# Performance work log

Hardware: AMD Instinct MI355X
Metric: run time of the kernel (lower is better)

## Reference

```python
import jax, jax.numpy as jnp
import numpy as np

N = 50000      # nodes
E = 600000     # edges
G = 512        # graphs in batch
H = 128        # hidden_dim
F_IN = 4       # node_features
ED = 2         # edge_dim
OUT = 256      # output_dim
L = 7          # conv layers 1..7 (layer 0 is separate: 4->128 with residual)
EPS = 1e-5     # BatchNorm eps


def setup_inputs() -> dict:
    key = jax.random.key(0)
    ks = jax.random.split(key, 32)
    rn = lambda k, shape, s=0.05: jax.random.normal(k, shape, dtype=jnp.float32) * s
    inp = {}
    inp["x"] = jax.random.normal(ks[0], (N, F_IN), dtype=jnp.float32)
    inp["edge_attr"] = jax.random.normal(ks[1], (E, ED), dtype=jnp.float32)
    # layer 0: EdgeUpdateConv(4, 128) with residual projection
    inp["We0"] = rn(ks[2], (F_IN + ED, H)); inp["be0"] = rn(ks[3], (H,))
    inp["Wn0"] = rn(ks[4], (H, H));        inp["bno0"] = rn(ks[5], (H,))
    inp["g0"] = jnp.ones((H,), jnp.float32); inp["bt0"] = jnp.zeros((H,), jnp.float32)
    inp["m0"] = rn(ks[6], (H,)); inp["v0"] = jax.random.uniform(ks[7], (H,), dtype=jnp.float32) + 0.5
    inp["Wr0"] = rn(ks[8], (F_IN, H)); inp["br0"] = rn(ks[9], (H,))
    # layers 1..7: EdgeUpdateConv(128, 128), stacked params
    inp["We_s"] = rn(ks[10], (L, H + ED, H)); inp["be_s"] = rn(ks[11], (L, H))
    inp["Wn_s"] = rn(ks[12], (L, H, H));      inp["bno_s"] = rn(ks[13], (L, H))
    inp["g_s"] = jnp.ones((L, H), jnp.float32); inp["bt_s"] = jnp.zeros((L, H), jnp.float32)
    inp["m_s"] = rn(ks[14], (L, H)); inp["v_s"] = jax.random.uniform(ks[15], (L, H), dtype=jnp.float32) + 0.5
    # head
    inp["W1"] = rn(ks[16], (2 * H, H)); inp["b1"] = rn(ks[17], (H,))
    inp["g1"] = jnp.ones((H,), jnp.float32); inp["bt1"] = jnp.zeros((H,), jnp.float32)
    inp["m1"] = rn(ks[18], (H,)); inp["v1"] = jax.random.uniform(ks[19], (H,), dtype=jnp.float32) + 0.5
    inp["W2"] = rn(ks[20], (H, OUT)); inp["b2"] = rn(ks[21], (OUT,))
    # int inputs
    inp["edge_index"] = jax.random.randint(ks[22], (2, E), 0, N, dtype=jnp.int32)
    inp["batch"] = jnp.sort(jax.random.randint(ks[23], (N,), 0, G, dtype=jnp.int32))
    return inp


def _bn(x, g, b, m, v):
    # eval-mode BatchNorm1d
    return (x - m) * (g * jax.lax.rsqrt(v + EPS)) + b


def reference(x, edge_attr, We0, be0, Wn0, bno0, g0, bt0, m0, v0, Wr0, br0,
              We_s, be_s, Wn_s, bno_s, g_s, bt_s, m_s, v_s,
              W1, b1, g1, bt1, m1, v1, W2, b2, edge_index, batch):
    src, dst = edge_index[0], edge_index[1]
    # in-degree for mean aggregation (isolated nodes -> 0 output, guard /0)
    deg = jnp.maximum(jax.ops.segment_sum(jnp.ones((E,), jnp.float32), dst, num_segments=N), 1.0)

    def conv(h, We, be, Wn, bno, g, bt, m, v, res):
        # message: gather x_j, concat edge_attr, linear_edge  -> [E, H]
        msg = jnp.concatenate([h[src], edge_attr], axis=1) @ We + be
        # scatter-mean aggregate -> [N, H]
        agg = jax.ops.segment_sum(msg, dst, num_segments=N) / deg[:, None]
        # update: linear_node, then BN, residual, ReLU
        out = _bn(agg @ Wn + bno, g, bt, m, v)
        return jax.nn.relu(out + res)

    h = conv(x, We0, be0, Wn0, bno0, g0, bt0, m0, v0, x @ Wr0 + br0)
    for i in range(L):  # fixed small layer loop
        h = conv(h, We_s[i], be_s[i], Wn_s[i], bno_s[i], g_s[i], bt_s[i], m_s[i], v_s[i], h)

    # global mean / max pooling per graph
    ones_n = jnp.ones((N,), jnp.float32)
    cnt = jnp.maximum(jax.ops.segment_sum(ones_n, batch, num_segments=G), 1.0)
    mean_p = jax.ops.segment_sum(h, batch, num_segments=G) / cnt[:, None]
    max_p = jax.ops.segment_max(h, batch, num_segments=G)
    z = jnp.concatenate([mean_p, max_p], axis=1)  # [G, 2H]
    z = jax.nn.relu(_bn(z @ W1 + b1, g1, bt1, m1, v1))
    z = z @ W2 + b2
    return z / jnp.maximum(jnp.linalg.norm(z, axis=1, keepdims=True), 1e-12)
```

## Files before the change

### kernel.cpp

```cpp
#include <hip/hip_runtime.h>

constexpr int NN   = 50000;
constexpr int NPAD = 50016;
constexpr int NE   = 600000;
constexpr int NG   = 512;
constexpr int HD   = 128;
constexpr float BN_EPS = 1e-5f;
constexpr int CWS  = HD*HD + 2*HD + HD;
constexpr int WMF_L = 2*4*4*128*8;

typedef __attribute__((ext_vector_type(8))) short bf16x8;
typedef __attribute__((ext_vector_type(4))) float f32x4;

__device__ inline unsigned short bf16rne(float v) {
  unsigned u = __float_as_uint(v);
  return (unsigned short)((u + 0x7FFFu + ((u >> 16) & 1u)) >> 16);
}
__device__ inline void bfsplit(float v, unsigned short& h, unsigned short& l) {
  unsigned short hb = bf16rne(v);
  float hf = __uint_as_float((unsigned)hb << 16);
  l = bf16rne(v - hf);
  h = hb;
}
__device__ inline float blo(unsigned u) { return __uint_as_float(u << 16); }
__device__ inline float bhi(unsigned u) { return __uint_as_float(u & 0xFFFF0000u); }


__global__ __launch_bounds__(256) void k_deg(const int* __restrict__ ei,
                                             int* __restrict__ deg, int* __restrict__ rank) {
  int e = blockIdx.x * 256 + threadIdx.x;
  if (e >= NE) return;
  rank[e] = atomicAdd(&deg[ei[NE + e]], 1);
}

__global__ __launch_bounds__(1024) void k_scanA(const int* __restrict__ deg,
                                                int* __restrict__ rowptr, int* __restrict__ bsum) {
  __shared__ int sm[1024];
  int t = threadIdx.x, b = blockIdx.x;
  int i = b * 1024 + t;
  int v = (i < NN) ? deg[i] : 0;
  sm[t] = v;
  __syncthreads();
  for (int off = 1; off < 1024; off <<= 1) {
    int add = (t >= off) ? sm[t - off] : 0;
    __syncthreads();
    sm[t] += add;
    __syncthreads();
  }
  int incl = sm[t];
  if (i < NN) rowptr[i] = incl - v;
  if (t == 1023) bsum[b] = incl;
}

__global__ __launch_bounds__(1024) void k_scanC(int* rowptr, const int* __restrict__ bsum) {
  __shared__ int base;
  int b = blockIdx.x;
  if (threadIdx.x == 0) {
    int acc = 0;
    for (int j = 0; j < b; j++) acc += bsum[j];
    base = acc;
    if (b == 0) rowptr[NN] = NE;
  }
  __syncthreads();
  int i = b * 1024 + threadIdx.x;
  if (i < NN) rowptr[i] += base;
}

__global__ __launch_bounds__(256) void k_scatter(
    const int* __restrict__ ei, const float* __restrict__ ea, const int* __restrict__ rowptr,
    const int* __restrict__ rank, int* __restrict__ csr, float* __restrict__ eap) {
  int e = blockIdx.x * 256 + threadIdx.x;
  if (e >= NE) return;
  int s = ei[e], d = ei[NE + e];
  int pos = rowptr[d] + rank[e];
  csr[pos] = s;
  *(float2*)(eap + 2 * (size_t)pos) = *(const float2*)(ea + 2 * (size_t)e);
}

__global__ __launch_bounds__(128) void k_combine(
    const float* __restrict__ We0, const float* __restrict__ be0, const float* __restrict__ Wn0,
    const float* __restrict__ We_s, const float* __restrict__ be_s, const float* __restrict__ Wn_s,
    float* __restrict__ cw, unsigned short* __restrict__ wmf) {
  int l = blockIdx.x / 131;
  int r = blockIdx.x % 131;
  int j = threadIdx.x;
  float* slot = cw + (size_t)l * CWS;
  const float* Wn;
  const float* Arow;
  float* dst;
  if (l == 0) {
    Wn = Wn0;
    if (r < 4)       { Arow = We0 + r * HD; dst = slot + r * HD; }
    else if (r < 6)  { Arow = We0 + r * HD; dst = slot + HD * HD + (r - 4) * HD; }
    else if (r == 6) { Arow = be0;          dst = slot + HD * HD + 2 * HD; }
    else return;
  } else {
    int li = l - 1;
    Wn = Wn_s + (size_t)li * HD * HD;
    const float* We = We_s + (size_t)li * 130 * HD;
    if (r < 128)      { Arow = We + r * HD;  dst = slot + r * HD; }
    else if (r < 130) { Arow = We + r * HD;  dst = slot + HD * HD + (r - 128) * HD; }
    else              { Arow = be_s + li * HD; dst = slot + HD * HD + 2 * HD; }
  }
  float acc = 0.f;
  for (int t = 0; t < HD; t++) acc = fmaf(Arow[t], Wn[t * HD + j], acc);
  dst[j] = acc;
  if (l >= 1 && r < 128) {
    unsigned short hb, lb;
    bfsplit(acc, hb, lb);
    size_t wbase = (size_t)(l - 1) * WMF_L;
    int kb = r >> 5, ks2 = (r >> 3) & 3, jj = r & 7;
    size_t o = (size_t)((kb * 4 + ks2) * 128 + j) * 8 + jj;
    wmf[wbase + o] = hb;
    wmf[wbase + WMF_L / 2 + o] = lb;
  }
}

__global__ __launch_bounds__(256) void k_node0(
    const int* __restrict__ rowptr, const int* __restrict__ csr, const float* __restrict__ eap,
    const float* __restrict__ x, const int* __restrict__ deg, const float* __restrict__ cw0,
    const float* __restrict__ bno0, const float* __restrict__ g0, const float* __restrict__ bt0,
    const float* __restrict__ m0, const float* __restrict__ v0,
    const float* __restrict__ Wr0, const float* __restrict__ br0,
    float* __restrict__ Se, unsigned short* __restrict__ outHi, unsigned short* __restrict__ outLo) {
  int g32 = threadIdx.x >> 5;
  int i = blockIdx.x * 8 + g32;
  if (i >= NN) return;
  int l = threadIdx.x & 31;
  int e0 = rowptr[i], e1 = rowptr[i + 1];
  float sx0 = 0.f, sx1 = 0.f, sx2 = 0.f, sx3 = 0.f, se0 = 0.f, se1 = 0.f;
  for (int e = e0 + l; e < e1; e += 32) {
    int s = csr[e];
    float4 xv = *(const float4*)(x + 4 * (size_t)s);
    sx0 += xv.x; sx1 += xv.y; sx2 += xv.z; sx3 += xv.w;
    float2 ev = *(const float2*)(eap + 2 * (size_t)e);
    se0 += ev.x; se1 += ev.y;
  }
#pragma unroll
  for (int m = 1; m <= 16; m <<= 1) {
    sx0 += __shfl_xor(sx0, m); sx1 += __shfl_xor(sx1, m);
    sx2 += __shfl_xor(sx2, m); sx3 += __shfl_xor(sx3, m);
    se0 += __shfl_xor(se0, m); se1 += __shfl_xor(se1, m);
  }
  if (l == 0) *(float2*)(Se + 2 * (size_t)i) = make_float2(se0, se1);
  float dg = (float)deg[i];
  float dgi = 1.0f / fmaxf(dg, 1.0f);
  float4 xr = *(const float4*)(x + 4 * (size_t)i);
  const float* Wc0  = cw0;
  const float* wce0 = cw0 + HD * HD;
  const float* bc0  = cw0 + HD * HD + 2 * HD;
  ushort4 hs, ls;
  unsigned short* hp = (unsigned short*)&hs;
  unsigned short* lp = (unsigned short*)&ls;
#pragma unroll
  for (int k2 = 0; k2 < 4; k2++) {
    int c = l * 4 + k2;
    float y = sx0 * Wc0[c] + sx1 * Wc0[HD + c] + sx2 * Wc0[2 * HD + c] + sx3 * Wc0[3 * HD + c];
    y += se0 * wce0[c] + se1 * wce0[HD + c] + dg * bc0[c];
    y = y * dgi + bno0[c];
    float sc = g0[c] * rsqrtf(v0[c] + BN_EPS);
    y = (y - m0[c]) * sc + bt0[c];
    float r = br0[c] + xr.x * Wr0[c] + xr.y * Wr0[HD + c] + xr.z * Wr0[2 * HD + c] + xr.w * Wr0[3 * HD + c];
    float o = fmaxf(y + r, 0.f);
    bfsplit(o, hp[k2], lp[k2]);
  }
  *(ushort4*)(outHi + (size_t)i * HD + l * 4) = hs;
  *(ushort4*)(outLo + (size_t)i * HD + l * 4) = ls;
}


__global__ __launch_bounds__(256, 8) void k_layer(
    const unsigned short* __restrict__ hHi, const unsigned short* __restrict__ hLo,
    const int* __restrict__ rowptr, const int* __restrict__ csr,
    const float* __restrict__ cwl, const unsigned short* __restrict__ wmf,
    const float* __restrict__ bno, const float* __restrict__ gam, const float* __restrict__ bet,
    const float* __restrict__ mu, const float* __restrict__ var,
    const float* __restrict__ Se, const int* __restrict__ deg,
    unsigned short* __restrict__ outHi, unsigned short* __restrict__ outLo) {
  __shared__ unsigned short St_hi[32 * 136];
  __shared__ unsigned short St_lo[32 * 136];
  int tid = threadIdx.x;
  int wid = tid >> 6, lane = tid & 63;
  int half = lane >> 5, l5 = lane & 31;
  int rowbase = blockIdx.x * 32;
  const uint2* hb2 = (const uint2*)hHi;

#pragma unroll
  for (int rp = 0; rp < 4; rp++) {
    int lr = wid * 8 + rp * 2 + half;
    int i = rowbase + lr;
    int e = 0, e1 = 0;
    if (i < NN) { e = rowptr[i]; e1 = rowptr[i + 1]; }
    float a0 = 0.f, a1 = 0.f, a2 = 0.f, a3 = 0.f;
    for (; e + 3 < e1; e += 4) {
      int s0 = csr[e], s1 = csr[e + 1], s2 = csr[e + 2], s3 = csr[e + 3];
      uint2 v0 = hb2[(size_t)s0 * 32 + l5];
      uint2 v1 = hb2[(size_t)s1 * 32 + l5];
      uint2 v2 = hb2[(size_t)s2 * 32 + l5];
      uint2 v3 = hb2[(size_t)s3 * 32 + l5];
      a0 += blo(v0.x) + blo(v1.x) + blo(v2.x) + blo(v3.x);
      a1 += bhi(v0.x) + bhi(v1.x) + bhi(v2.x) + bhi(v3.x);
      a2 += blo(v0.y) + blo(v1.y) + blo(v2.y) + blo(v3.y);
      a3 += bhi(v0.y) + bhi(v1.y) + bhi(v2.y) + bhi(v3.y);
    }
    if (e + 1 < e1) {
      int s0 = csr[e], s1 = csr[e + 1];
      uint2 v0 = hb2[(size_t)s0 * 32 + l5];
      uint2 v1 = hb2[(size_t)s1 * 32 + l5];
      a0 += blo(v0.x) + blo(v1.x); a1 += bhi(v0.x) + bhi(v1.x);
      a2 += blo(v0.y) + blo(v1.y); a3 += bhi(v0.y) + bhi(v1.y);
      e += 2;
    }
    if (e < e1) {
      uint2 v = hb2[(size_t)csr[e] * 32 + l5];
      a0 += blo(v.x); a1 += bhi(v.x); a2 += blo(v.y); a3 += bhi(v.y);
    }
    unsigned short h0, l0, h1, l1, h2, l2, h3, l3;
    bfsplit(a0, h0, l0); bfsplit(a1, h1, l1); bfsplit(a2, h2, l2); bfsplit(a3, h3, l3);
    *(ushort4*)&St_hi[lr * 136 + l5 * 4] = make_ushort4(h0, h1, h2, h3);
    *(ushort4*)&St_lo[lr * 136 + l5 * 4] = make_ushort4(l0, l1, l2, l3);
  }
  __syncthreads();

  int wm = wid >> 1, wn = wid & 1;
  int nlane = lane & 15, ksub = lane >> 4;
  const unsigned short* wh = wmf;
  const unsigned short* wl = wmf + WMF_L / 2;
  f32x4 acc[4];
#pragma unroll
  for (int nt = 0; nt < 4; nt++) acc[nt] = (f32x4){0.f, 0.f, 0.f, 0.f};
  int arow = wm * 16 + nlane;
#pragma unroll
  for (int ks = 0; ks < 4; ks++) {
    bf16x8 ah = *(const bf16x8*)&St_hi[arow * 136 + ks * 32 + ksub * 8];
    bf16x8 al = *(const bf16x8*)&St_lo[arow * 136 + ks * 32 + ksub * 8];
#pragma unroll
    for (int nt = 0; nt < 4; nt++) {
      int col = wn * 64 + nt * 16 + nlane;
      bf16x8 bh = *(const bf16x8*)&wh[(size_t)((ks * 4 + ksub) * 128 + col) * 8];
      bf16x8 bl = *(const bf16x8*)&wl[(size_t)((ks * 4 + ksub) * 128 + col) * 8];
      acc[nt] = __builtin_amdgcn_mfma_f32_16x16x32_bf16(ah, bh, acc[nt], 0, 0, 0);
      acc[nt] = __builtin_amdgcn_mfma_f32_16x16x32_bf16(al, bh, acc[nt], 0, 0, 0);
      acc[nt] = __builtin_amdgcn_mfma_f32_16x16x32_bf16(ah, bl, acc[nt], 0, 0, 0);
    }
  }

  const float* wce = cwl + HD * HD;
  const float* bcp = cwl + HD * HD + 2 * HD;
  int rb = wm * 16 + ksub * 4;
  float dgv[4], dgiv[4];
  float2 sevv[4];
#pragma unroll
  for (int i2 = 0; i2 < 4; i2++) {
    size_t row = (size_t)rowbase + rb + i2;
    float dg = (float)deg[row];
    dgv[i2] = dg;
    dgiv[i2] = 1.0f / fmaxf(dg, 1.0f);
    sevv[i2] = *(const float2*)(Se + row * 2);
  }
#pragma unroll
  for (int nt = 0; nt < 4; nt++) {
    int col = wn * 64 + nt * 16 + nlane;
    float w0 = wce[col], w1 = wce[HD + col], bcv = bcp[col], bnov = bno[col];
    float sc = gam[col] * rsqrtf(var[col] + BN_EPS);
    float sh = bet[col] - mu[col] * sc;
#pragma unroll
    for (int i2 = 0; i2 < 4; i2++) {
      size_t row = (size_t)rowbase + rb + i2;
      size_t idx = row * HD + col;
      float res = __uint_as_float((unsigned)hHi[idx] << 16)
                + __uint_as_float((unsigned)hLo[idx] << 16);
      float y = (acc[nt][i2] + sevv[i2].x * w0 + sevv[i2].y * w1 + dgv[i2] * bcv) * dgiv[i2] + bnov;
      y = fmaxf(y * sc + sh + res, 0.f);
      unsigned short yh, yl;
      bfsplit(y, yh, yl);
      outHi[idx] = yh;
      outLo[idx] = yl;
    }
  }
}


__global__ __launch_bounds__(512) void k_pool(
    const unsigned short* __restrict__ hb, const int* __restrict__ batch,
    float* __restrict__ meanp, float* __restrict__ maxp) {
  __shared__ float ssum[512], smax[512];
  int g = blockIdx.x, t = threadIdx.x;
  int d = t & 127, sub = t >> 7;
  int lo = 0, hi = NN;
  while (lo < hi) { int mid = (lo + hi) >> 1; if (batch[mid] < g) lo = mid + 1; else hi = mid; }
  int start = lo;
  lo = start; hi = NN;
  while (lo < hi) { int mid = (lo + hi) >> 1; if (batch[mid] < g + 1) lo = mid + 1; else hi = mid; }
  int end = lo;
  float sum = 0.f, mx = -3.4e38f;
  for (int i = start + sub; i < end; i += 4) {
    float val = __uint_as_float((unsigned)hb[(size_t)i * HD + d] << 16);
    sum += val;
    mx = fmaxf(mx, val);
  }
  ssum[t] = sum; smax[t] = mx;
  __syncthreads();
  if (sub == 0) {
    sum = ssum[t] + ssum[t + 128] + ssum[t + 256] + ssum[t + 384];
    mx = fmaxf(fmaxf(smax[t], smax[t + 128]), fmaxf(smax[t + 256], smax[t + 384]));
    int cnt = end - start;
    meanp[g * HD + d] = sum / fmaxf((float)cnt, 1.f);
    maxp[g * HD + d] = (cnt > 0) ? mx : 0.f;
  }
}

__global__ __launch_bounds__(256) void k_head(
    const float* __restrict__ meanp, const float* __restrict__ maxp,
    const float* __restrict__ W1, const float* __restrict__ b1,
    const float* __restrict__ g1, const float* __restrict__ bt1,
    const float* __restrict__ m1, const float* __restrict__ v1,
    const float* __restrict__ W2, const float* __restrict__ b2,
    float* __restrict__ outp) {
  __shared__ float z[256];
  __shared__ float s1[128];
  __shared__ float red[256];
  int g = blockIdx.x, t = threadIdx.x;
  z[t] = (t < 128) ? meanp[g * HD + t] : maxp[g * HD + (t - 128)];
  __syncthreads();
  if (t < 128) {
    float y = b1[t];
    for (int k = 0; k < 256; k++) y = fmaf(z[k], W1[k * HD + t], y);
    float sc = g1[t] * rsqrtf(v1[t] + BN_EPS);
    y = (y - m1[t]) * sc + bt1[t];
    s1[t] = fmaxf(y, 0.f);
  }
  __syncthreads();
  float o = b2[t];
  for (int k = 0; k < 128; k++) o = fmaf(s1[k], W2[k * 256 + t], o);
  red[t] = o * o;
  __syncthreads();
  for (int off = 128; off > 0; off >>= 1) {
    if (t < off) red[t] += red[t + off];
    __syncthreads();
  }
  float scale = 1.0f / fmaxf(sqrtf(red[0]), 1e-12f);
  outp[(size_t)g * 256 + t] = o * scale;
}


extern "C" void kernel_launch(void* const* d_in, const int* in_sizes, int n_in,
                              void* d_out, int out_size, void* d_ws, size_t ws_size,
                              hipStream_t stream) {
  const float* x         = (const float*)d_in[0];
  const float* edge_attr = (const float*)d_in[1];
  const float* We0  = (const float*)d_in[2];
  const float* be0  = (const float*)d_in[3];
  const float* Wn0  = (const float*)d_in[4];
  const float* bno0 = (const float*)d_in[5];
  const float* g0   = (const float*)d_in[6];
  const float* bt0  = (const float*)d_in[7];
  const float* m0   = (const float*)d_in[8];
  const float* v0   = (const float*)d_in[9];
  const float* Wr0  = (const float*)d_in[10];
  const float* br0  = (const float*)d_in[11];
  const float* We_s = (const float*)d_in[12];
  const float* be_s = (const float*)d_in[13];
  const float* Wn_s = (const float*)d_in[14];
  const float* bno_s= (const float*)d_in[15];
  const float* g_s  = (const float*)d_in[16];
  const float* bt_s = (const float*)d_in[17];
  const float* m_s  = (const float*)d_in[18];
  const float* v_s  = (const float*)d_in[19];
  const float* W1   = (const float*)d_in[20];
  const float* b1   = (const float*)d_in[21];
  const float* g1   = (const float*)d_in[22];
  const float* bt1  = (const float*)d_in[23];
  const float* m1   = (const float*)d_in[24];
  const float* v1   = (const float*)d_in[25];
  const float* W2   = (const float*)d_in[26];
  const float* b2   = (const float*)d_in[27];
  const int* edge_index = (const int*)d_in[28];
  const int* batch      = (const int*)d_in[29];
  float* outp = (float*)d_out;

  char* ws = (char*)d_ws;
  size_t off = 0;
  auto alloc = [&](size_t bytes) -> void* {
    void* p = ws + off;
    off = (off + bytes + 255) & ~(size_t)255;
    return p;
  };
  unsigned short* hAHi = (unsigned short*)alloc((size_t)NPAD * HD * 2);
  unsigned short* hALo = (unsigned short*)alloc((size_t)NPAD * HD * 2);
  unsigned short* hBHi = (unsigned short*)alloc((size_t)NPAD * HD * 2);
  unsigned short* hBLo = (unsigned short*)alloc((size_t)NPAD * HD * 2);
  float* Se    = (float*)alloc((size_t)NPAD * 2 * 4);
  int*   deg   = (int*)alloc((size_t)NPAD * 4);
  int*   rowptr= (int*)alloc((size_t)(NN + 1) * 4);
  int*   rank  = (int*)alloc((size_t)NE * 4);
  int*   csr   = (int*)alloc((size_t)NE * 4);
  float* eap   = (float*)alloc((size_t)NE * 2 * 4);
  int*   bsum  = (int*)alloc(64 * 4);
  float* cw    = (float*)alloc((size_t)8 * CWS * 4);
  unsigned short* wmf = (unsigned short*)alloc((size_t)7 * WMF_L * 2);
  float* meanp = (float*)alloc((size_t)NG * HD * 4);
  float* maxp  = (float*)alloc((size_t)NG * HD * 4);
  (void)ws_size; (void)n_in; (void)in_sizes; (void)out_size;

  hipMemsetAsync(deg, 0, (size_t)NPAD * 4, stream);

  k_deg<<<(NE + 255) / 256, 256, 0, stream>>>(edge_index, deg, rank);
  k_scanA<<<49, 1024, 0, stream>>>(deg, rowptr, bsum);
  k_scanC<<<49, 1024, 0, stream>>>(rowptr, bsum);
  k_scatter<<<(NE + 255) / 256, 256, 0, stream>>>(edge_index, edge_attr, rowptr, rank, csr, eap);
  k_combine<<<8 * 131, 128, 0, stream>>>(We0, be0, Wn0, We_s, be_s, Wn_s, cw, wmf);
  k_node0<<<(NN + 7) / 8, 256, 0, stream>>>(rowptr, csr, eap, x, deg, cw,
                                            bno0, g0, bt0, m0, v0, Wr0, br0,
                                            Se, hAHi, hALo);

  unsigned short* curHi = hAHi; unsigned short* curLo = hALo;
  unsigned short* othHi = hBHi; unsigned short* othLo = hBLo;
  for (int l = 1; l <= 7; ++l) {
    int li = l - 1;
    k_layer<<<NPAD / 32, 256, 0, stream>>>(curHi, curLo, rowptr, csr,
        cw + (size_t)l * CWS, wmf + (size_t)li * WMF_L,
        bno_s + li * HD, g_s + li * HD, bt_s + li * HD, m_s + li * HD, v_s + li * HD,
        Se, deg, othHi, othLo);
    unsigned short* t;
    t = curHi; curHi = othHi; othHi = t;
    t = curLo; curLo = othLo; othLo = t;
  }

  k_pool<<<NG, 512, 0, stream>>>(curHi, batch, meanp, maxp);
  k_head<<<NG, 256, 0, stream>>>(meanp, maxp, W1, b1, g1, bt1, m1, v1, W2, b2, outp);
}
```

Baseline: 538.0 us.

## Halve layer tile rows, fuse deg with combine and pool with head

The layer kernel now processes 16 rows per block instead of 32. Each of the four waves owns a 32-column slice of a single 16-row MFMA tile, which doubles the block count to improve load balance on the gather phase. The degree-count kernel and the weight-combine kernel are merged into one launch, and pooling is merged with the MLP head, removing two launches and the intermediate mean/max buffers. The trade-off is that each block reloads the weight fragments for fewer rows, so weight reuse per block drops.

```diff
diff --git a/kernel.cpp b/kernel.cpp
--- a/kernel.cpp
+++ b/kernel.cpp
@@ -8,6 +8,10 @@
 constexpr float BN_EPS = 1e-5f;
 constexpr int CWS  = HD*HD + 2*HD + HD;
 constexpr int WMF_L = 2*4*4*128*8;
+constexpr int TR   = 16;
+constexpr int DEG_BLOCKS = (NE + 255) / 256;
+constexpr int CMB_UNITS  = 8 * 131;
+constexpr int CMB_BLOCKS = CMB_UNITS / 2;
 
 typedef __attribute__((ext_vector_type(8))) short bf16x8;
 typedef __attribute__((ext_vector_type(4))) float f32x4;
@@ -26,64 +30,19 @@
 __device__ inline float bhi(unsigned u) { return __uint_as_float(u & 0xFFFF0000u); }
 
 
-__global__ __launch_bounds__(256) void k_deg(const int* __restrict__ ei,
-                                             int* __restrict__ deg, int* __restrict__ rank) {
-  int e = blockIdx.x * 256 + threadIdx.x;
-  if (e >= NE) return;
-  rank[e] = atomicAdd(&deg[ei[NE + e]], 1);
-}
-
-__global__ __launch_bounds__(1024) void k_scanA(const int* __restrict__ deg,
-                                                int* __restrict__ rowptr, int* __restrict__ bsum) {
-  __shared__ int sm[1024];
-  int t = threadIdx.x, b = blockIdx.x;
-  int i = b * 1024 + t;
-  int v = (i < NN) ? deg[i] : 0;
-  sm[t] = v;
-  __syncthreads();
-  for (int off = 1; off < 1024; off <<= 1) {
-    int add = (t >= off) ? sm[t - off] : 0;
-    __syncthreads();
-    sm[t] += add;
-    __syncthreads();
-  }
-  int incl = sm[t];
-  if (i < NN) rowptr[i] = incl - v;
-  if (t == 1023) bsum[b] = incl;
-}
-
-__global__ __launch_bounds__(1024) void k_scanC(int* rowptr, const int* __restrict__ bsum) {
-  __shared__ int base;
-  int b = blockIdx.x;
-  if (threadIdx.x == 0) {
-    int acc = 0;
-    for (int j = 0; j < b; j++) acc += bsum[j];
-    base = acc;
-    if (b == 0) rowptr[NN] = NE;
-  }
-  __syncthreads();
-  int i = b * 1024 + threadIdx.x;
-  if (i < NN) rowptr[i] += base;
-}
-
-__global__ __launch_bounds__(256) void k_scatter(
-    const int* __restrict__ ei, const float* __restrict__ ea, const int* __restrict__ rowptr,
-    const int* __restrict__ rank, int* __restrict__ csr, float* __restrict__ eap) {
-  int e = blockIdx.x * 256 + threadIdx.x;
-  if (e >= NE) return;
-  int s = ei[e], d = ei[NE + e];
-  int pos = rowptr[d] + rank[e];
-  csr[pos] = s;
-  *(float2*)(eap + 2 * (size_t)pos) = *(const float2*)(ea + 2 * (size_t)e);
-}
-
-__global__ __launch_bounds__(128) void k_combine(
+__global__ __launch_bounds__(256) void k_deg_combine(
+    const int* __restrict__ ei, int* __restrict__ deg, int* __restrict__ rank,
     const float* __restrict__ We0, const float* __restrict__ be0, const float* __restrict__ Wn0,
     const float* __restrict__ We_s, const float* __restrict__ be_s, const float* __restrict__ Wn_s,
     float* __restrict__ cw, unsigned short* __restrict__ wmf) {
-  int l = blockIdx.x / 131;
-  int r = blockIdx.x % 131;
-  int j = threadIdx.x;
+  int b = blockIdx.x;
+  if (b < DEG_BLOCKS) {
+    int e = b * 256 + threadIdx.x;
+    if (e < NE) rank[e] = atomicAdd(&deg[ei[NE + e]], 1);
+    return;
+  }
+  int u = (b - DEG_BLOCKS) * 2 + (threadIdx.x >> 7);
+  int l = u / 131, r = u % 131, j = threadIdx.x & 127;
   float* slot = cw + (size_t)l * CWS;
   const float* Wn;
   const float* Arow;
@@ -114,6 +73,51 @@
     wmf[wbase + o] = hb;
     wmf[wbase + WMF_L / 2 + o] = lb;
   }
+}
+
+
+__global__ __launch_bounds__(1024) void k_scanA(const int* __restrict__ deg,
+                                                int* __restrict__ rowptr, int* __restrict__ bsum) {
+  __shared__ int sm[1024];
+  int t = threadIdx.x, b = blockIdx.x;
+  int i = b * 1024 + t;
+  int v = (i < NN) ? deg[i] : 0;
+  sm[t] = v;
+  __syncthreads();
+  for (int off = 1; off < 1024; off <<= 1) {
+    int add = (t >= off) ? sm[t - off] : 0;
+    __syncthreads();
+    sm[t] += add;
+    __syncthreads();
+  }
+  int incl = sm[t];
+  if (i < NN) rowptr[i] = incl - v;
+  if (t == 1023) bsum[b] = incl;
+}
+
+__global__ __launch_bounds__(1024) void k_scanC(int* rowptr, const int* __restrict__ bsum) {
+  __shared__ int base;
+  int b = blockIdx.x;
+  if (threadIdx.x == 0) {
+    int acc = 0;
+    for (int j = 0; j < b; j++) acc += bsum[j];
+    base = acc;
+    if (b == 0) rowptr[NN] = NE;
+  }
+  __syncthreads();
+  int i = b * 1024 + threadIdx.x;
+  if (i < NN) rowptr[i] += base;
+}
+
+__global__ __launch_bounds__(256) void k_scatter(
+    const int* __restrict__ ei, const float* __restrict__ ea, const int* __restrict__ rowptr,
+    const int* __restrict__ rank, int* __restrict__ csr, float* __restrict__ eap) {
+  int e = blockIdx.x * 256 + threadIdx.x;
+  if (e >= NE) return;
+  int s = ei[e], d = ei[NE + e];
+  int pos = rowptr[d] + rank[e];
+  csr[pos] = s;
+  *(float2*)(eap + 2 * (size_t)pos) = *(const float2*)(ea + 2 * (size_t)e);
 }
 
 __global__ __launch_bounds__(256) void k_node0(
@@ -177,17 +181,17 @@
     const float* __restrict__ mu, const float* __restrict__ var,
     const float* __restrict__ Se, const int* __restrict__ deg,
     unsigned short* __restrict__ outHi, unsigned short* __restrict__ outLo) {
-  __shared__ unsigned short St_hi[32 * 136];
-  __shared__ unsigned short St_lo[32 * 136];
+  __shared__ unsigned short St_hi[TR * 136];
+  __shared__ unsigned short St_lo[TR * 136];
   int tid = threadIdx.x;
   int wid = tid >> 6, lane = tid & 63;
   int half = lane >> 5, l5 = lane & 31;
-  int rowbase = blockIdx.x * 32;
+  int rowbase = blockIdx.x * TR;
   const uint2* hb2 = (const uint2*)hHi;
 
 #pragma unroll
-  for (int rp = 0; rp < 4; rp++) {
-    int lr = wid * 8 + rp * 2 + half;
+  for (int rp = 0; rp < 2; rp++) {
+    int lr = wid * 4 + rp * 2 + half;
     int i = rowbase + lr;
     int e = 0, e1 = 0;
     if (i < NN) { e = rowptr[i]; e1 = rowptr[i + 1]; }
@@ -222,21 +226,19 @@
   }
   __syncthreads();
 
-  int wm = wid >> 1, wn = wid & 1;
   int nlane = lane & 15, ksub = lane >> 4;
   const unsigned short* wh = wmf;
   const unsigned short* wl = wmf + WMF_L / 2;
-  f32x4 acc[4];
-#pragma unroll
-  for (int nt = 0; nt < 4; nt++) acc[nt] = (f32x4){0.f, 0.f, 0.f, 0.f};
-  int arow = wm * 16 + nlane;
+  f32x4 acc[2];
+#pragma unroll
+  for (int nt = 0; nt < 2; nt++) acc[nt] = (f32x4){0.f, 0.f, 0.f, 0.f};
 #pragma unroll
   for (int ks = 0; ks < 4; ks++) {
-    bf16x8 ah = *(const bf16x8*)&St_hi[arow * 136 + ks * 32 + ksub * 8];
-    bf16x8 al = *(const bf16x8*)&St_lo[arow * 136 + ks * 32 + ksub * 8];
-#pragma unroll
-    for (int nt = 0; nt < 4; nt++) {
-      int col = wn * 64 + nt * 16 + nlane;
+    bf16x8 ah = *(const bf16x8*)&St_hi[nlane * 136 + ks * 32 + ksub * 8];
+    bf16x8 al = *(const bf16x8*)&St_lo[nlane * 136 + ks * 32 + ksub * 8];
+#pragma unroll
+    for (int nt = 0; nt < 2; nt++) {
+      int col = wid * 32 + nt * 16 + nlane;
       bf16x8 bh = *(const bf16x8*)&wh[(size_t)((ks * 4 + ksub) * 128 + col) * 8];
       bf16x8 bl = *(const bf16x8*)&wl[(size_t)((ks * 4 + ksub) * 128 + col) * 8];
       acc[nt] = __builtin_amdgcn_mfma_f32_16x16x32_bf16(ah, bh, acc[nt], 0, 0, 0);
@@ -247,7 +249,7 @@
 
   const float* wce = cwl + HD * HD;
   const float* bcp = cwl + HD * HD + 2 * HD;
-  int rb = wm * 16 + ksub * 4;
+  int rb = ksub * 4;
   float dgv[4], dgiv[4];
   float2 sevv[4];
 #pragma unroll
@@ -259,8 +261,8 @@
     sevv[i2] = *(const float2*)(Se + row * 2);
   }
 #pragma unroll
-  for (int nt = 0; nt < 4; nt++) {
-    int col = wn * 64 + nt * 16 + nlane;
+  for (int nt = 0; nt < 2; nt++) {
+    int col = wid * 32 + nt * 16 + nlane;
     float w0 = wce[col], w1 = wce[HD + col], bcv = bcp[col], bnov = bno[col];
     float sc = gam[col] * rsqrtf(var[col] + BN_EPS);
     float sh = bet[col] - mu[col] * sc;
@@ -281,10 +283,17 @@
 }
 
 
-__global__ __launch_bounds__(512) void k_pool(
+__global__ __launch_bounds__(512) void k_poolhead(
     const unsigned short* __restrict__ hb, const int* __restrict__ batch,
-    float* __restrict__ meanp, float* __restrict__ maxp) {
+    const float* __restrict__ W1, const float* __restrict__ b1,
+    const float* __restrict__ g1, const float* __restrict__ bt1,
+    const float* __restrict__ m1, const float* __restrict__ v1,
+    const float* __restrict__ W2, const float* __restrict__ b2,
+    float* __restrict__ outp) {
   __shared__ float ssum[512], smax[512];
+  __shared__ float pmean[128], pmax[128];
+  __shared__ float s1[128];
+  __shared__ float red[512];
   int g = blockIdx.x, t = threadIdx.x;
   int d = t & 127, sub = t >> 7;
   int lo = 0, hi = NN;
@@ -305,42 +314,32 @@
     sum = ssum[t] + ssum[t + 128] + ssum[t + 256] + ssum[t + 384];
     mx = fmaxf(fmaxf(smax[t], smax[t + 128]), fmaxf(smax[t + 256], smax[t + 384]));
     int cnt = end - start;
-    meanp[g * HD + d] = sum / fmaxf((float)cnt, 1.f);
-    maxp[g * HD + d] = (cnt > 0) ? mx : 0.f;
-  }
-}
-
-__global__ __launch_bounds__(256) void k_head(
-    const float* __restrict__ meanp, const float* __restrict__ maxp,
-    const float* __restrict__ W1, const float* __restrict__ b1,
-    const float* __restrict__ g1, const float* __restrict__ bt1,
-    const float* __restrict__ m1, const float* __restrict__ v1,
-    const float* __restrict__ W2, const float* __restrict__ b2,
-    float* __restrict__ outp) {
-  __shared__ float z[256];
-  __shared__ float s1[128];
-  __shared__ float red[256];
-  int g = blockIdx.x, t = threadIdx.x;
-  z[t] = (t < 128) ? meanp[g * HD + t] : maxp[g * HD + (t - 128)];
+    pmean[d] = sum / fmaxf((float)cnt, 1.f);
+    pmax[d] = (cnt > 0) ? mx : 0.f;
+  }
   __syncthreads();
   if (t < 128) {
     float y = b1[t];
-    for (int k = 0; k < 256; k++) y = fmaf(z[k], W1[k * HD + t], y);
+    for (int k = 0; k < 128; k++) y = fmaf(pmean[k], W1[k * HD + t], y);
+    for (int k = 0; k < 128; k++) y = fmaf(pmax[k], W1[(128 + k) * HD + t], y);
     float sc = g1[t] * rsqrtf(v1[t] + BN_EPS);
     y = (y - m1[t]) * sc + bt1[t];
     s1[t] = fmaxf(y, 0.f);
   }
   __syncthreads();
-  float o = b2[t];
-  for (int k = 0; k < 128; k++) o = fmaf(s1[k], W2[k * 256 + t], o);
+  float o = 0.f;
+  if (t < 256) {
+    o = b2[t];
+    for (int k = 0; k < 128; k++) o = fmaf(s1[k], W2[k * 256 + t], o);
+  }
   red[t] = o * o;
   __syncthreads();
-  for (int off = 128; off > 0; off >>= 1) {
+  for (int off = 256; off > 0; off >>= 1) {
     if (t < off) red[t] += red[t + off];
     __syncthreads();
   }
   float scale = 1.0f / fmaxf(sqrtf(red[0]), 1e-12f);
-  outp[(size_t)g * 256 + t] = o * scale;
+  if (t < 256) outp[(size_t)g * 256 + t] = o * scale;
 }
 
 
@@ -399,17 +398,15 @@
   int*   bsum  = (int*)alloc(64 * 4);
   float* cw    = (float*)alloc((size_t)8 * CWS * 4);
   unsigned short* wmf = (unsigned short*)alloc((size_t)7 * WMF_L * 2);
-  float* meanp = (float*)alloc((size_t)NG * HD * 4);
-  float* maxp  = (float*)alloc((size_t)NG * HD * 4);
   (void)ws_size; (void)n_in; (void)in_sizes; (void)out_size;
 
   hipMemsetAsync(deg, 0, (size_t)NPAD * 4, stream);
 
-  k_deg<<<(NE + 255) / 256, 256, 0, stream>>>(edge_index, deg, rank);
+  k_deg_combine<<<DEG_BLOCKS + CMB_BLOCKS, 256, 0, stream>>>(
+      edge_index, deg, rank, We0, be0, Wn0, We_s, be_s, Wn_s, cw, wmf);
   k_scanA<<<49, 1024, 0, stream>>>(deg, rowptr, bsum);
   k_scanC<<<49, 1024, 0, stream>>>(rowptr, bsum);
   k_scatter<<<(NE + 255) / 256, 256, 0, stream>>>(edge_index, edge_attr, rowptr, rank, csr, eap);
-  k_combine<<<8 * 131, 128, 0, stream>>>(We0, be0, Wn0, We_s, be_s, Wn_s, cw, wmf);
   k_node0<<<(NN + 7) / 8, 256, 0, stream>>>(rowptr, csr, eap, x, deg, cw,
                                             bno0, g0, bt0, m0, v0, Wr0, br0,
                                             Se, hAHi, hALo);
@@ -418,7 +415,7 @@
   unsigned short* othHi = hBHi; unsigned short* othLo = hBLo;
   for (int l = 1; l <= 7; ++l) {
     int li = l - 1;
-    k_layer<<<NPAD / 32, 256, 0, stream>>>(curHi, curLo, rowptr, csr,
+    k_layer<<<NPAD / TR, 256, 0, stream>>>(curHi, curLo, rowptr, csr,
         cw + (size_t)l * CWS, wmf + (size_t)li * WMF_L,
         bno_s + li * HD, g_s + li * HD, bt_s + li * HD, m_s + li * HD, v_s + li * HD,
         Se, deg, othHi, othLo);
@@ -427,6 +424,5 @@
     t = curLo; curLo = othLo; othLo = t;
   }
 
-  k_pool<<<NG, 512, 0, stream>>>(curHi, batch, meanp, maxp);
-  k_head<<<NG, 256, 0, stream>>>(meanp, maxp, W1, b1, g1, bt1, m1, v1, W2, b2, outp);
-}
+  k_poolhead<<<NG, 512, 0, stream>>>(curHi, batch, W1, b1, g1, bt1, m1, v1, W2, b2, outp);
+}
```

Result: faster. 485.5 us (-9.8%).
